# Kernel tuning notes

Hardware: AMD Instinct MI355X
Metric: run time of the kernel (lower is better)

The kernel has to match this reference:

```python
import jax, jax.numpy as jnp
import numpy as np
import math

FEATURE_DIM = 512
QK_DIM = 256
EPS = 1e-12  # torch F.normalize eps


def _l2norm(x):
    n = jnp.linalg.norm(x, axis=-1, keepdims=True)
    return x / jnp.maximum(n, EPS)


def setup_inputs() -> dict:
    key = jax.random.key(0)
    ks = jax.random.split(key, 6)
    B, Nq, Nk = 16, 2048, 2048
    query = jax.random.normal(ks[0], (B, Nq, FEATURE_DIM), dtype=jnp.float32)
    key_t = jax.random.normal(ks[1], (B, Nk, FEATURE_DIM // 2), dtype=jnp.float32)
    value = jax.random.normal(ks[2], (B, Nk, FEATURE_DIM // 2), dtype=jnp.float32)
    # weights stored torch-style [out, in], init N(0, sqrt(2/out))
    WQ = jax.random.normal(ks[3], (QK_DIM, FEATURE_DIM), dtype=jnp.float32) * math.sqrt(2.0 / QK_DIM)
    WK = jax.random.normal(ks[4], (QK_DIM, FEATURE_DIM // 2), dtype=jnp.float32) * math.sqrt(2.0 / QK_DIM)
    WV = jax.random.normal(ks[5], (FEATURE_DIM, FEATURE_DIM // 2), dtype=jnp.float32) * math.sqrt(2.0 / FEATURE_DIM)
    return {"query": query, "key": key_t, "value": value, "WQ": WQ, "WK": WK, "WV": WV}


def reference(query, key, value, WQ, WK, WV):
    temp = QK_DIM ** (-0.5)
    w_q = _l2norm(jnp.einsum('bnf,qf->bnq', query, WQ))      # [B, Nq, D]
    w_k = _l2norm(jnp.einsum('bmf,qf->bmq', key, WK))        # [B, Nk, D]
    dot = jnp.einsum('bnd,bmd->bnm', w_q, w_k)               # cosine sims
    affinity = jax.nn.softmax(dot * temp, axis=-1)
    w_v = _l2norm(jnp.einsum('bmf,vf->bmv', value, WV))      # [B, Nk, F]
    out = jnp.einsum('bnm,bmv->bnv', affinity, w_v)
    return out + query
```

## Files before the change

kernel.cpp:

```cpp
#include <hip/hip_runtime.h>

typedef float        f32x4  __attribute__((ext_vector_type(4)));
typedef float        f32x16 __attribute__((ext_vector_type(16)));
typedef unsigned int u32x4  __attribute__((ext_vector_type(4)));
typedef unsigned int u32x2  __attribute__((ext_vector_type(2)));
typedef int          i32x2  __attribute__((ext_vector_type(2)));
typedef __bf16       bf16x8 __attribute__((ext_vector_type(8)));

#define DEVFN static __device__ __forceinline__

DEVFN unsigned cvtpk(float a, float b){
  unsigned r;
  asm("v_cvt_pk_bf16_f32 %0, %1, %2" : "=v"(r) : "v"(a), "v"(b));
  return r;
}
DEVFN float exp2_hw(float x){
  float r;
  asm("v_exp_f32 %0, %1" : "=v"(r) : "v"(x));
  return r;
}
DEVFN bf16x8 as_bf(u32x4 v){ union{u32x4 u; bf16x8 b;} x; x.u=v; return x.b; }

DEVFN unsigned char f2fp8(float v){
  int r = __builtin_amdgcn_cvt_pk_fp8_f32(v, v, 0, false);
  return (unsigned char)(r & 0xff);
}
DEVFN unsigned pk4_fp8(float a, float b, float c, float d){
  int r = __builtin_amdgcn_cvt_pk_fp8_f32(a, b, 0, false);
  r = __builtin_amdgcn_cvt_pk_fp8_f32(c, d, r, true);
  return (unsigned)r;
}
DEVFN long mk64(unsigned lo, unsigned hi){
  return (long)(((unsigned long long)hi << 32) | lo);
}

DEVFN void gload16(const char* src, char* lds){
  __builtin_amdgcn_global_load_lds(
      (__attribute__((address_space(1))) void*)src,
      (__attribute__((address_space(3))) void*)lds, 16, 0, 0);
}

constexpr int BB = 16, NQ = 2048, NK = 2048, F = 512, D = 256, FV = 512;

template<int KD, int ND, int MODE>
__global__ __launch_bounds__(256,2) void proj_kernel(const float* __restrict__ X,
                                                     const float* __restrict__ W,
                                                     unsigned char* __restrict__ Y,
                                                     float scale)
{
  constexpr bool TR = (MODE == 2);
  constexpr int NW = ND/4;
  constexpr int AF = TR ? 8 : 2;
  constexpr int BF = TR ? 2 : NW/16;
  __shared__ __align__(16) char xsm[32*80];
  __shared__ __align__(16) char wsm[ND*80];
  __shared__ float wsum[4][32];
  const int tid = threadIdx.x;
  const int lane = tid & 63;
  const int wid = tid >> 6;
  const int q16 = lane & 15;
  const int g = lane >> 4;
  const int row0 = blockIdx.x * 32;
  const int rX = tid >> 3, cX = (tid & 7) * 4;

  f32x4 z4 = {0.f,0.f,0.f,0.f};
  f32x4 acc[AF][BF];
  #pragma unroll
  for (int i=0;i<AF;i++){
    #pragma unroll
    for (int j=0;j<BF;j++) acc[i][j] = z4;
  }

  f32x4 xr = *(const f32x4*)(X + (size_t)(row0+rX)*KD + cX);
  f32x4 wr[ND/32];
  #pragma unroll
  for (int j=0;j<ND/32;j++)
    wr[j] = *(const f32x4*)(W + (size_t)(j*32+rX)*KD + cX);

  for (int k0 = 0; k0 < KD; k0 += 32){
    {
      u32x2 p; p[0]=cvtpk(xr[0],xr[1]); p[1]=cvtpk(xr[2],xr[3]);
      *(u32x2*)(xsm + rX*80 + cX*2) = p;
    }
    #pragma unroll
    for (int j=0;j<ND/32;j++){
      u32x2 p; p[0]=cvtpk(wr[j][0],wr[j][1]); p[1]=cvtpk(wr[j][2],wr[j][3]);
      *(u32x2*)(wsm + (j*32+rX)*80 + cX*2) = p;
    }
    if (k0 + 32 < KD){
      xr = *(const f32x4*)(X + (size_t)(row0+rX)*KD + k0+32 + cX);
      #pragma unroll
      for (int j=0;j<ND/32;j++)
        wr[j] = *(const f32x4*)(W + (size_t)(j*32+rX)*KD + k0+32 + cX);
    }
    __syncthreads();
    if constexpr (!TR){
      bf16x8 a[2], bb[BF];
      #pragma unroll
      for (int mi=0;mi<2;mi++)  a[mi]  = as_bf(*(const u32x4*)(xsm + (16*mi+q16)*80 + g*16));
      #pragma unroll
      for (int ni=0;ni<BF;ni++) bb[ni] = as_bf(*(const u32x4*)(wsm + (wid*NW + 16*ni + q16)*80 + g*16));
      #pragma unroll
      for (int mi=0;mi<2;mi++){
        #pragma unroll
        for (int ni=0;ni<BF;ni++)
          acc[mi][ni] = __builtin_amdgcn_mfma_f32_16x16x32_bf16(a[mi], bb[ni], acc[mi][ni], 0,0,0);
      }
    } else {
      bf16x8 a[8], bb[2];
      #pragma unroll
      for (int ai=0;ai<8;ai++) a[ai] = as_bf(*(const u32x4*)(wsm + (wid*NW + 16*ai + q16)*80 + g*16));
      #pragma unroll
      for (int ci=0;ci<2;ci++) bb[ci] = as_bf(*(const u32x4*)(xsm + (16*ci+q16)*80 + g*16));
      #pragma unroll
      for (int ai=0;ai<8;ai++){
        #pragma unroll
        for (int ci=0;ci<2;ci++)
          acc[ai][ci] = __builtin_amdgcn_mfma_f32_16x16x32_bf16(a[ai], bb[ci], acc[ai][ci], 0,0,0);
      }
    }
    __syncthreads();
  }

  if constexpr (!TR){
    float part[2][4];
    #pragma unroll
    for (int mi=0;mi<2;mi++){
      #pragma unroll
      for (int r=0;r<4;r++){
        float s=0.f;
        #pragma unroll
        for (int ni=0;ni<BF;ni++){ float v=acc[mi][ni][r]; s += v*v; }
        part[mi][r]=s;
      }
    }
    #pragma unroll
    for (int m=1;m<16;m<<=1){
      #pragma unroll
      for (int mi=0;mi<2;mi++){
        #pragma unroll
        for (int r=0;r<4;r++) part[mi][r] += __shfl_xor(part[mi][r], m);
      }
    }
    if (q16 == 0){
      #pragma unroll
      for (int mi=0;mi<2;mi++){
        #pragma unroll
        for (int r=0;r<4;r++) wsum[wid][16*mi + 4*g + r] = part[mi][r];
      }
    }
    __syncthreads();
    #pragma unroll
    for (int mi=0;mi<2;mi++){
      #pragma unroll
      for (int r=0;r<4;r++){
        int m = 16*mi + 4*g + r;
        float tot = wsum[0][m]+wsum[1][m]+wsum[2][m]+wsum[3][m];
        float inv = scale / fmaxf(sqrtf(tot), 1e-12f);
        int row = row0 + m;
        #pragma unroll
        for (int ni=0;ni<BF;ni++){
          int col = wid*NW + 16*ni + q16;
          unsigned char vb = f2fp8(acc[mi][ni][r]*inv);
          if constexpr (MODE == 0){
            Y[(size_t)row*ND + col] = vb;
          } else {
            int b2 = row >> 11, kv = row & 2047;
            int kt = kv >> 5, mm = kv & 31;
            int u = col >> 5, dd = col & 31;
            int s = ((dd>>4)<<3) | (dd&7);
            int l = mm + ((dd>>3)&1)*32;
            Y[((((size_t)b2*64 + kt)*8 + u)*64 + l)*16 + s] = vb;
          }
        }
      }
    }
  } else {
    float pp[2];
    #pragma unroll
    for (int ci=0;ci<2;ci++){
      float s=0.f;
      #pragma unroll
      for (int ai=0;ai<8;ai++){
        #pragma unroll
        for (int r=0;r<4;r++){ float v=acc[ai][ci][r]; s += v*v; }
      }
      pp[ci]=s;
    }
    #pragma unroll
    for (int ci=0;ci<2;ci++){
      pp[ci] += __shfl_xor(pp[ci],16);
      pp[ci] += __shfl_xor(pp[ci],32);
    }
    if (lane < 16){ wsum[wid][lane] = pp[0]; wsum[wid][16+lane] = pp[1]; }
    __syncthreads();
    #pragma unroll
    for (int ci=0;ci<2;ci++){
      int m = 16*ci + q16;
      float tot = wsum[0][m]+wsum[1][m]+wsum[2][m]+wsum[3][m];
      float inv = scale / fmaxf(sqrtf(tot), 1e-12f);
      int grow = row0 + m;
      int b2 = grow >> 11;
      int kv = grow & 2047;
      int kt = kv >> 5, kl = kv & 31;
      int s = ((kl>>4)<<3) | (kl&7);
      int lofs = ((kl>>3)&1)*32;
      #pragma unroll
      for (int ai=0;ai<8;ai++){
        #pragma unroll
        for (int r=0;r<4;r++){
          int n = wid*NW + 16*ai + 4*g + r;
          int fvh = n >> 8, u = (n>>5)&7, mm = n & 31;
          unsigned char vb = f2fp8(acc[ai][ci][r]*inv);
          Y[(((((size_t)b2*64 + kt)*2 + fvh)*8 + u)*64 + (mm + lofs))*16 + s] = vb;
        }
      }
    }
  }
}

__global__ __launch_bounds__(512,2) void attn_kernel(const float* __restrict__ query,
    const unsigned char* __restrict__ wq8, const unsigned char* __restrict__ k8,
    const unsigned char* __restrict__ v8, float* __restrict__ out)
{
  __shared__ __align__(16) char smem[106496];
  const int tid = threadIdx.x, lane = tid & 63, wid = tid >> 6;
  const int l31 = lane & 31, h = lane >> 5;
  const int qs = wid & 3, fvh = wid >> 2;
  const int bid = blockIdx.x;
  const int lb = (bid & 7)*32 + (bid >> 3);
  const int b = lb >> 4;
  const int qblk = lb & 15;
  const int q0 = qblk*128;

  const char* ksrc = (const char*)(k8 + (size_t)b*524288)  + lane*16;
  const char* vsrc = (const char*)(v8 + (size_t)b*1048576) + lane*16;
  char* const pwav = smem + 98304 + qs*2048;

  #define STAGE(T, CUR) do{                                                  \
    gload16(ksrc + (size_t)(T)*16384 + (2*wid  )*1024,                       \
            smem + (CUR)*16384 + (2*wid  )*1024);                            \
    gload16(ksrc + (size_t)(T)*16384 + (2*wid+1)*1024,                       \
            smem + (CUR)*16384 + (2*wid+1)*1024);                            \
    _Pragma("unroll")                                                        \
    for (int i_=0;i_<4;i_++)                                                 \
      gload16(vsrc + (size_t)(T)*32768 + (4*wid+i_)*1024,                    \
              smem + 32768 + (CUR)*32768 + (4*wid+i_)*1024);                 \
  }while(0)

  STAGE(0, 0);

  unsigned long long qf[16];
  {
    const unsigned char* qb = wq8 + ((size_t)b*NQ + q0 + qs*32 + l31)*D;
    #pragma unroll
    for (int c=0;c<16;c++) qf[c] = *(const unsigned long long*)(qb + c*16 + h*8);
  }

  f32x16 z16;
  #pragma unroll
  for (int i=0;i<16;i++) z16[i]=0.f;
  f32x16 o[8];
  #pragma unroll
  for (int i=0;i<8;i++) o[i]=z16;
  float ssum = 0.f;
  const float c2 = 0.0625f * 1.4426950408889634f / 64.0f;

  __syncthreads();

  #define BODY(T, CUR) do{                                                          \
    if ((T) < 31) STAGE((T)+1, (CUR)^1);                                            \
                                         \
    const char* kb = smem + (CUR)*16384 + fvh*8192;                                 \
    f32x16 S = z16;                                                                 \
    __builtin_amdgcn_s_setprio(1);                                                  \
    _Pragma("unroll")                                                               \
    for (int u=0;u<8;u++){                                                          \
      u32x4 kk = *(const u32x4*)(kb + u*1024 + lane*16);                            \
      S = __builtin_amdgcn_mfma_f32_32x32x16_fp8_fp8(mk64(kk[0],kk[1]),             \
            (long)qf[2*u],   S, 0,0,0);                                             \
      S = __builtin_amdgcn_mfma_f32_32x32x16_fp8_fp8(mk64(kk[2],kk[3]),             \
            (long)qf[2*u+1], S, 0,0,0);                                             \
    }                                                                               \
    __builtin_amdgcn_s_setprio(0);                                                  \
    float p[16];                                                                    \
    _Pragma("unroll")                                                               \
    for (int r=0;r<16;r++) p[r] = exp2_hw(S[r]*c2);                                 \
    {                                                                               \
      float s2a = (p[0]+p[1])+(p[2]+p[3]),  s2b = (p[4]+p[5])+(p[6]+p[7]);          \
      float s2c = (p[8]+p[9])+(p[10]+p[11]), s2d = (p[12]+p[13])+(p[14]+p[15]);     \
      ssum += (s2a+s2b) + (s2c+s2d);                                                \
    }                                                                               \
                \
    _Pragma("unroll")                                                               \
    for (int m=0;m<4;m++){                                                          \
      unsigned dw = pk4_fp8(p[4*m],p[4*m+1],p[4*m+2],p[4*m+3]);                     \
      *(unsigned*)(pwav + fvh*1024 + (m*2+h)*128 + l31*4) = dw;                     \
    }                                                                               \
    __syncthreads();                 \
    __builtin_amdgcn_s_setprio(1);                                                  \
    _Pragma("unroll")                                                               \
    for (int s=0;s<2;s++){                                                          \
                  \
      unsigned lo0 = *(const unsigned*)(pwav + s*1024 + ((0+h)*2  )*128 + l31*4);   \
      unsigned hi0 = *(const unsigned*)(pwav + s*1024 + ((0+h)*2+1)*128 + l31*4);   \
      unsigned lo1 = *(const unsigned*)(pwav + s*1024 + ((2+h)*2  )*128 + l31*4);   \
      unsigned hi1 = *(const unsigned*)(pwav + s*1024 + ((2+h)*2+1)*128 + l31*4);   \
      long B0 = mk64(lo0, hi0), B1 = mk64(lo1, hi1);                                \
      const char* vb = smem + 32768 + (CUR)*32768 + s*16384 + fvh*8192;             \
      _Pragma("unroll")                                                             \
      for (int u=0;u<8;u++){                                                        \
        u32x4 vv = *(const u32x4*)(vb + u*1024 + lane*16);                          \
        o[u] = __builtin_amdgcn_mfma_f32_32x32x16_fp8_fp8(mk64(vv[0],vv[1]), B0,    \
                                                          o[u], 0,0,0);             \
        o[u] = __builtin_amdgcn_mfma_f32_32x32x16_fp8_fp8(mk64(vv[2],vv[3]), B1,    \
                                                          o[u], 0,0,0);             \
      }                                                                             \
    }                                                                               \
    __builtin_amdgcn_s_setprio(0);                                                  \
    __syncthreads();                   \
  }while(0)

  for (int tt = 0; tt < 32; tt += 2){
    BODY(tt,   0);
    BODY(tt+1, 1);
  }
  #undef BODY
  #undef STAGE

  ssum += __shfl_xor(ssum, 32);
  {
    float* sx = (float*)(smem + 98304);
    sx[(qs*2+fvh)*32 + l31] = ssum;
    __syncthreads();
    ssum += sx[(qs*2+(1-fvh))*32 + l31];
  }
  const float inv = 1.f/(8.f*ssum);
  #pragma unroll
  for (int i=0;i<8;i++){
    #pragma unroll
    for (int r=0;r<16;r++) o[i][r] *= inv;
  }

  char* wsc = smem + qs*16384;
  union U16 { f32x16 v; f32x4 q4[4]; };
  const int swz = (l31 & 7) << 4;
  #pragma unroll
  for (int phase=0; phase<2; ++phase){
    if (fvh == phase){
      #pragma unroll
      for (int hf=0; hf<2; ++hf){
        #pragma unroll
        for (int fc2=0; fc2<4; ++fc2){
          U16 u; u.v = o[hf*4+fc2];
          #pragma unroll
          for (int k=0;k<4;k++){
            *(f32x4*)(wsc + l31*512 + ((fc2*128 + k*32 + h*16) ^ swz)) = u.q4[k];
          }
        }
        #pragma unroll
        for (int p2=0;p2<16;p2++){
          int qr = p2*2 + h;
          f32x4 v = *(const f32x4*)(wsc + qr*512 + ((l31*16) ^ ((qr&7)<<4)));
          size_t row = (size_t)b*NQ + q0 + qs*32 + qr;
          int col = fvh*256 + hf*128 + l31*4;
          f32x4 qv = *(const f32x4*)(query + row*F + col);
          #pragma unroll
          for (int e=0;e<4;e++) v[e] += qv[e];
          *(f32x4*)(out + row*F + col) = v;
        }
      }
    }
    __syncthreads();
  }
}

extern "C" void kernel_launch(void* const* d_in, const int* in_sizes, int n_in,
                              void* d_out, int out_size, void* d_ws, size_t ws_size,
                              hipStream_t stream)
{
  const float* query = (const float*)d_in[0];
  const float* key   = (const float*)d_in[1];
  const float* value = (const float*)d_in[2];
  const float* WQ    = (const float*)d_in[3];
  const float* WK    = (const float*)d_in[4];
  const float* WV    = (const float*)d_in[5];
  float* out = (float*)d_out;

  unsigned char* wq8 = (unsigned char*)d_ws;
  unsigned char* k8  = wq8 + (size_t)BB*NQ*D;
  unsigned char* v8  = k8  + (size_t)BB*NK*D;

  dim3 blk(256);
  proj_kernel<512,256,0><<<1024, blk, 0, stream>>>(query, WQ, wq8, 8.0f);
  proj_kernel<256,256,1><<<1024, blk, 0, stream>>>(key,   WK, k8,  8.0f);
  proj_kernel<256,512,2><<<1024, blk, 0, stream>>>(value, WV, v8,  8.0f);
  attn_kernel<<<256, dim3(512), 0, stream>>>(query, wq8, k8, v8, out);
}
```

Measured before the change: 172.1 us.

## Fuse three projection kernels into one launch with double-buffered LDS

Merges the Q, K and V projection kernels into a single 3072-block launch that dispatches on block index, removing two kernel launches and the gaps between them. For the non-transposed modes the LDS staging is double-buffered by iteration parity, which drops the trailing barrier per k-step. The shared LDS allocation is sized for the largest case (46 KB), which may reduce occupancy for the smaller modes, and an extra barrier is added before the wsum write.

New measurement: 163.2 us. 5.2% less time.

```diff
diff --git a/kernel.cpp b/kernel.cpp
--- a/kernel.cpp
+++ b/kernel.cpp
@@ -43,24 +43,21 @@
 constexpr int BB = 16, NQ = 2048, NK = 2048, F = 512, D = 256, FV = 512;
 
 template<int KD, int ND, int MODE>
-__global__ __launch_bounds__(256,2) void proj_kernel(const float* __restrict__ X,
-                                                     const float* __restrict__ W,
-                                                     unsigned char* __restrict__ Y,
-                                                     float scale)
+DEVFN void proj_body(const float* __restrict__ X, const float* __restrict__ W,
+                     unsigned char* __restrict__ Y, float scale,
+                     char* sm, float (*wsum)[32], int bid)
 {
   constexpr bool TR = (MODE == 2);
   constexpr int NW = ND/4;
   constexpr int AF = TR ? 8 : 2;
   constexpr int BF = TR ? 2 : NW/16;
-  __shared__ __align__(16) char xsm[32*80];
-  __shared__ __align__(16) char wsm[ND*80];
-  __shared__ float wsum[4][32];
+  constexpr int NIT = KD/32;
   const int tid = threadIdx.x;
   const int lane = tid & 63;
   const int wid = tid >> 6;
   const int q16 = lane & 15;
   const int g = lane >> 4;
-  const int row0 = blockIdx.x * 32;
+  const int row0 = bid * 32;
   const int rX = tid >> 3, cX = (tid & 7) * 4;
 
   f32x4 z4 = {0.f,0.f,0.f,0.f};
@@ -77,29 +74,33 @@
   for (int j=0;j<ND/32;j++)
     wr[j] = *(const f32x4*)(W + (size_t)(j*32+rX)*KD + cX);
 
-  for (int k0 = 0; k0 < KD; k0 += 32){
+  for (int t = 0; t < NIT; ++t){
+    char* xb; char* wb;
+    if constexpr (TR){ xb = sm; wb = sm + 2560; }
+    else { xb = sm + (t&1)*23040; wb = xb + 2560; }
     {
       u32x2 p; p[0]=cvtpk(xr[0],xr[1]); p[1]=cvtpk(xr[2],xr[3]);
-      *(u32x2*)(xsm + rX*80 + cX*2) = p;
+      *(u32x2*)(xb + rX*80 + cX*2) = p;
     }
     #pragma unroll
     for (int j=0;j<ND/32;j++){
       u32x2 p; p[0]=cvtpk(wr[j][0],wr[j][1]); p[1]=cvtpk(wr[j][2],wr[j][3]);
-      *(u32x2*)(wsm + (j*32+rX)*80 + cX*2) = p;
-    }
-    if (k0 + 32 < KD){
-      xr = *(const f32x4*)(X + (size_t)(row0+rX)*KD + k0+32 + cX);
+      *(u32x2*)(wb + (j*32+rX)*80 + cX*2) = p;
+    }
+    if (t + 1 < NIT){
+      int k0n = (t+1)*32;
+      xr = *(const f32x4*)(X + (size_t)(row0+rX)*KD + k0n + cX);
       #pragma unroll
       for (int j=0;j<ND/32;j++)
-        wr[j] = *(const f32x4*)(W + (size_t)(j*32+rX)*KD + k0+32 + cX);
+        wr[j] = *(const f32x4*)(W + (size_t)(j*32+rX)*KD + k0n + cX);
     }
     __syncthreads();
     if constexpr (!TR){
       bf16x8 a[2], bb[BF];
       #pragma unroll
-      for (int mi=0;mi<2;mi++)  a[mi]  = as_bf(*(const u32x4*)(xsm + (16*mi+q16)*80 + g*16));
-      #pragma unroll
-      for (int ni=0;ni<BF;ni++) bb[ni] = as_bf(*(const u32x4*)(wsm + (wid*NW + 16*ni + q16)*80 + g*16));
+      for (int mi=0;mi<2;mi++)  a[mi]  = as_bf(*(const u32x4*)(xb + (16*mi+q16)*80 + g*16));
+      #pragma unroll
+      for (int ni=0;ni<BF;ni++) bb[ni] = as_bf(*(const u32x4*)(wb + (wid*NW + 16*ni + q16)*80 + g*16));
       #pragma unroll
       for (int mi=0;mi<2;mi++){
         #pragma unroll
@@ -109,17 +110,17 @@
     } else {
       bf16x8 a[8], bb[2];
       #pragma unroll
-      for (int ai=0;ai<8;ai++) a[ai] = as_bf(*(const u32x4*)(wsm + (wid*NW + 16*ai + q16)*80 + g*16));
-      #pragma unroll
-      for (int ci=0;ci<2;ci++) bb[ci] = as_bf(*(const u32x4*)(xsm + (16*ci+q16)*80 + g*16));
+      for (int ai=0;ai<8;ai++) a[ai] = as_bf(*(const u32x4*)(wb + (wid*NW + 16*ai + q16)*80 + g*16));
+      #pragma unroll
+      for (int ci=0;ci<2;ci++) bb[ci] = as_bf(*(const u32x4*)(xb + (16*ci+q16)*80 + g*16));
       #pragma unroll
       for (int ai=0;ai<8;ai++){
         #pragma unroll
         for (int ci=0;ci<2;ci++)
           acc[ai][ci] = __builtin_amdgcn_mfma_f32_16x16x32_bf16(a[ai], bb[ci], acc[ai][ci], 0,0,0);
       }
-    }
-    __syncthreads();
+      __syncthreads();
+    }
   }
 
   if constexpr (!TR){
@@ -142,6 +143,7 @@
         for (int r=0;r<4;r++) part[mi][r] += __shfl_xor(part[mi][r], m);
       }
     }
+    __syncthreads();
     if (q16 == 0){
       #pragma unroll
       for (int mi=0;mi<2;mi++){
@@ -216,6 +218,25 @@
         }
       }
     }
+  }
+}
+
+__global__ __launch_bounds__(256,2) void proj_all(
+    const float* __restrict__ query, const float* __restrict__ key,
+    const float* __restrict__ value, const float* __restrict__ WQ,
+    const float* __restrict__ WK, const float* __restrict__ WV,
+    unsigned char* __restrict__ wq8, unsigned char* __restrict__ k8,
+    unsigned char* __restrict__ v8, float sq)
+{
+  __shared__ __align__(16) char sm[46080];
+  __shared__ float wsum[4][32];
+  const int bid = blockIdx.x;
+  if (bid < 1024){
+    proj_body<512,256,0>(query, WQ, wq8, sq,   sm, wsum, bid);
+  } else if (bid < 2048){
+    proj_body<256,256,1>(key,   WK, k8,  8.0f, sm, wsum, bid - 1024);
+  } else {
+    proj_body<256,512,2>(value, WV, v8,  8.0f, sm, wsum, bid - 2048);
   }
 }
 
@@ -301,7 +322,6 @@
     __builtin_amdgcn_s_setprio(1);                                                  \
     _Pragma("unroll")                                                               \
     for (int s=0;s<2;s++){                                                          \
-                  \
       unsigned lo0 = *(const unsigned*)(pwav + s*1024 + ((0+h)*2  )*128 + l31*4);   \
       unsigned hi0 = *(const unsigned*)(pwav + s*1024 + ((0+h)*2+1)*128 + l31*4);   \
       unsigned lo1 = *(const unsigned*)(pwav + s*1024 + ((2+h)*2  )*128 + l31*4);   \
@@ -391,9 +411,7 @@
   unsigned char* k8  = wq8 + (size_t)BB*NQ*D;
   unsigned char* v8  = k8  + (size_t)BB*NK*D;
 
-  dim3 blk(256);
-  proj_kernel<512,256,0><<<1024, blk, 0, stream>>>(query, WQ, wq8, 8.0f);
-  proj_kernel<256,256,1><<<1024, blk, 0, stream>>>(key,   WK, k8,  8.0f);
-  proj_kernel<256,512,2><<<1024, blk, 0, stream>>>(value, WV, v8,  8.0f);
+  proj_all<<<3072, dim3(256), 0, stream>>>(query, key, value, WQ, WK, WV,
+                                           wq8, k8, v8, 8.0f);
   attn_kernel<<<256, dim3(512), 0, stream>>>(query, wq8, k8, v8, out);
 }
```
